# Kernel tuning notes

Measured on AMD Instinct MI355X. Metric: run time of the kernel, lower is better.

The kernel has to match this reference:

```python
import jax, jax.numpy as jnp
import numpy as np

EMB = 4096   # emb_size for c2=256 (per TransformerEncoderBlock mapping)
HEADS = 16
HDIM = EMB // HEADS  # 256
N = 25               # (h // (h//5))**2 patches
PATCH = 4            # h//5 with h=20
C = 256
HW = 20
LN_EPS = 1e-5


def _layernorm(x, g, b):
    m = jnp.mean(x, axis=-1, keepdims=True)
    v = jnp.var(x, axis=-1, keepdims=True)
    return (x - m) * jax.lax.rsqrt(v + LN_EPS) * g + b


def setup_inputs() -> dict:
    key = jax.random.key(0)
    ks = jax.random.split(key, 14)
    s = 0.02
    rn = lambda k, shape, sc=s: jax.random.normal(k, shape, jnp.float32) * sc
    return {
        "x": jax.random.normal(ks[0], (1, C, HW, HW), jnp.float32),
        # PatchEmbedding: Conv2d(C, EMB, k=4, s=4) + positions
        "pe_w": rn(ks[1], (EMB, C, PATCH, PATCH)),
        "pe_b": jnp.zeros((EMB,), jnp.float32),
        "pos": rn(ks[2], (N, EMB), 1.0),  # nn.Parameter(torch.randn(...))
        # shared LayerNorm (same module used twice per block)
        "ln_g": jnp.ones((EMB,), jnp.float32),
        "ln_b": jnp.zeros((EMB,), jnp.float32),
        # attention
        "qkv_w": rn(ks[3], (EMB, 3 * EMB)),
        "qkv_b": jnp.zeros((3 * EMB,), jnp.float32),
        "proj_w": rn(ks[4], (EMB, EMB)),
        "proj_b": jnp.zeros((EMB,), jnp.float32),
        # FFN (expansion 4)
        "ff1_w": rn(ks[5], (EMB, 4 * EMB)),
        "ff1_b": jnp.zeros((4 * EMB,), jnp.float32),
        "ff2_w": rn(ks[6], (4 * EMB, EMB)),
        "ff2_b": jnp.zeros((EMB,), jnp.float32),
    }


def _forward(x, pe_w, pe_b, pos, ln_g, ln_b, qkv_w, qkv_b, proj_w, proj_b,
             ff1_w, ff1_b, ff2_w, ff2_b):
    b = x.shape[0]
    # Patch embedding: Conv2d(k=4, s=4) -> [b, EMB, 5, 5] -> [b, 25, EMB]
    t = jax.lax.conv_general_dilated(
        x, pe_w, window_strides=(PATCH, PATCH), padding="VALID",
        dimension_numbers=("NCHW", "OIHW", "NCHW"))
    t = t + pe_b[None, :, None, None]
    t = t.reshape(b, EMB, N).transpose(0, 2, 1) + pos  # [b, N, EMB]

    # --- TransformerEncoderBlock (dropout inactive / eval mode) ---
    # attention branch
    h = _layernorm(t, ln_g, ln_b)
    qkv = (h @ qkv_w + qkv_b).reshape(b, N, HEADS, HDIM, 3)  # (h d qkv) split
    q = qkv[..., 0].transpose(0, 2, 1, 3)  # [b, H, N, D]
    k = qkv[..., 1].transpose(0, 2, 1, 3)
    v = qkv[..., 2].transpose(0, 2, 1, 3)
    energy = jnp.einsum("bhqd,bhkd->bhqk", q, k)
    # NOTE: original scales AFTER softmax by sqrt(emb_size) -- faithful copy
    att = jax.nn.softmax(energy, axis=-1) / (EMB ** 0.5)
    o = jnp.einsum("bhqk,bhkd->bhqd", att, v)
    o = o.transpose(0, 2, 1, 3).reshape(b, N, EMB)
    t = t + (o @ proj_w + proj_b)

    # FFN branch (same shared layernorm params)
    h = _layernorm(t, ln_g, ln_b)
    h = jax.nn.gelu(h @ ff1_w + ff1_b, approximate=False)  # torch nn.GELU exact
    t = t + (h @ ff2_w + ff2_b)

    # final reshape(1, c2, w, h)
    return t.reshape(1, C, HW, HW)


def reference(x, pe_w, pe_b, pos, ln_g, ln_b, qkv_w, qkv_b, proj_w, proj_b,
              ff1_w, ff1_b, ff2_w, ff2_b):
    return _forward(x, pe_w, pe_b, pos, ln_g, ln_b, qkv_w, qkv_b, proj_w,
                    proj_b, ff1_w, ff1_b, ff2_w, ff2_b)
```

## Files before the change

kernel.cpp:

```cpp
#include <hip/hip_runtime.h>
#include <math.h>

#define TOK 25

typedef __attribute__((ext_vector_type(8))) short short8_t;
typedef __attribute__((ext_vector_type(4))) float f32x4_t;

__device__ __forceinline__ short bf16r(float f) {
  union { float f; unsigned u; } v;
  v.f = f;
  unsigned r = v.u + 0x7FFFu + ((v.u >> 16) & 1u);
  return (short)(r >> 16);
}
__device__ __forceinline__ unsigned packbf2(float lo, float hi) {
  return ((unsigned)(unsigned short)bf16r(hi) << 16) |
         (unsigned short)bf16r(lo);
}

__global__ __launch_bounds__(256) void k_patchify(const float* __restrict__ x,
                                                  unsigned short* __restrict__ P) {
  int idx = blockIdx.x * 256 + threadIdx.x;
  int n = idx >> 12;
  int rem = idx & 4095;
  int c = rem >> 4;
  int kh = (rem >> 2) & 3;
  int kw = rem & 3;
  int py = n / 5, px = n - py * 5;
  P[idx] = (unsigned short)bf16r(x[c * 400 + (py * 4 + kh) * 20 + (px * 4 + kw)]);
}

template <int KC, int WT>
__global__ __launch_bounds__(256) void k_mfma(
    const unsigned short* __restrict__ A, const float* __restrict__ W,
    float* __restrict__ part, int K, int N) {
  constexpr int LDA = KC + 8;
  __shared__ __align__(16) unsigned short As[TOK * LDA];
  const int tid = threadIdx.x;
  const int lane = tid & 63;
  const int lm = lane & 15;
  const int lg = lane >> 4;
  const int wv = tid >> 6;
  const int s = blockIdx.y;
  const int k0 = s * KC;
  const int c0 = blockIdx.x * 256 + wv * 64;
  for (int i = tid; i < TOK * (KC / 8); i += 256) {
    int r = i / (KC / 8);
    int o = i - r * (KC / 8);
    uint4 v = *reinterpret_cast<const uint4*>(A + (long)r * K + k0 + o * 8);
    *reinterpret_cast<uint4*>(&As[r * LDA + o * 8]) = v;
  }
  __syncthreads();
  const int r1 = 16 + lm;
  const int r1c = (r1 < TOK) ? r1 : 0;
  f32x4_t acc[4][2];
#pragma unroll
  for (int g = 0; g < 4; ++g) {
    acc[g][0] = (f32x4_t){0.f, 0.f, 0.f, 0.f};
    acc[g][1] = (f32x4_t){0.f, 0.f, 0.f, 0.f};
  }
  for (int ks = 0; ks < KC; ks += 32) {
    const int kb = k0 + ks + lg * 8;
    float bf[4][8];
    if (WT == 0) {
      const float* bp = W + (long)kb * N + c0 + lm;
#pragma unroll
      for (int j = 0; j < 8; ++j) {
        const float* bj = bp + (long)j * N;
#pragma unroll
        for (int g = 0; g < 4; ++g) bf[g][j] = bj[g * 16];
      }
    } else {
#pragma unroll
      for (int g = 0; g < 4; ++g) {
        const float* bp = W + (long)(c0 + g * 16 + lm) * K + kb;
        float4 b0 = *reinterpret_cast<const float4*>(bp);
        float4 b1 = *reinterpret_cast<const float4*>(bp + 4);
        bf[g][0] = b0.x; bf[g][1] = b0.y; bf[g][2] = b0.z; bf[g][3] = b0.w;
        bf[g][4] = b1.x; bf[g][5] = b1.y; bf[g][6] = b1.z; bf[g][7] = b1.w;
      }
    }
    short8_t av0 =
        *reinterpret_cast<const short8_t*>(&As[lm * LDA + ks + lg * 8]);
    short8_t av1 =
        *reinterpret_cast<const short8_t*>(&As[r1c * LDA + ks + lg * 8]);
#pragma unroll
    for (int g = 0; g < 4; ++g) {
      short8_t bv;
#pragma unroll
      for (int j = 0; j < 8; ++j) bv[j] = bf16r(bf[g][j]);
      acc[g][0] = __builtin_amdgcn_mfma_f32_16x16x32_bf16(av0, bv, acc[g][0], 0, 0, 0);
      acc[g][1] = __builtin_amdgcn_mfma_f32_16x16x32_bf16(av1, bv, acc[g][1], 0, 0, 0);
    }
  }
  float* pp = part + ((long)s * TOK) * N + c0 + lm;
#pragma unroll
  for (int g = 0; g < 4; ++g) {
    float* pg = pp + g * 16;
#pragma unroll
    for (int r = 0; r < 4; ++r) {
      int row0 = lg * 4 + r;
      pg[(long)row0 * N] = acc[g][0][r];
      int row1 = 16 + lg * 4 + r;
      if (row1 < TOK) pg[(long)row1 * N] = acc[g][1][r];
    }
  }
}

template <int S, int GELU, int RES, int OBF>
__global__ __launch_bounds__(256) void k_reduce(const float* __restrict__ part,
                                                const float* __restrict__ bias,
                                                const float* __restrict__ res,
                                                void* __restrict__ outv,
                                                int Nout) {
  long idx4 = (long)blockIdx.x * 256 + threadIdx.x;
  int c4 = (int)(idx4 % (Nout >> 2));
  const long stride4 = (long)TOK * (Nout >> 2);
  const float4* p4 = reinterpret_cast<const float4*>(part) + idx4;
  float4 v = {0.f, 0.f, 0.f, 0.f};
#pragma unroll
  for (int s = 0; s < S; ++s) {
    float4 t = p4[s * stride4];
    v.x += t.x; v.y += t.y; v.z += t.z; v.w += t.w;
  }
  float4 bb = reinterpret_cast<const float4*>(bias)[c4];
  v.x += bb.x; v.y += bb.y; v.z += bb.z; v.w += bb.w;
  if (GELU) {
    v.x = 0.5f * v.x * (1.f + erff(v.x * 0.70710678118654752f));
    v.y = 0.5f * v.y * (1.f + erff(v.y * 0.70710678118654752f));
    v.z = 0.5f * v.z * (1.f + erff(v.z * 0.70710678118654752f));
    v.w = 0.5f * v.w * (1.f + erff(v.w * 0.70710678118654752f));
  }
  if (RES) {
    float4 rr = reinterpret_cast<const float4*>(res)[idx4];
    v.x += rr.x; v.y += rr.y; v.z += rr.z; v.w += rr.w;
  }
  if (OBF) {
    uint2 o;
    o.x = packbf2(v.x, v.y);
    o.y = packbf2(v.z, v.w);
    reinterpret_cast<uint2*>(outv)[idx4] = o;
  } else {
    reinterpret_cast<float4*>(outv)[idx4] = v;
  }
}

__global__ __launch_bounds__(256) void k_ln(const float* __restrict__ t,
                                            const float* __restrict__ g,
                                            const float* __restrict__ b,
                                            unsigned short* __restrict__ h) {
  const int n = blockIdx.x;
  const float4* row = reinterpret_cast<const float4*>(t + n * 4096);
  float s = 0.f, s2 = 0.f;
  float4 vbuf[4];
#pragma unroll
  for (int it = 0; it < 4; ++it) {
    float4 v = row[threadIdx.x + it * 256];
    vbuf[it] = v;
    s += v.x + v.y + v.z + v.w;
    s2 += v.x * v.x + v.y * v.y + v.z * v.z + v.w * v.w;
  }
#pragma unroll
  for (int off = 32; off >= 1; off >>= 1) {
    s += __shfl_down(s, off);
    s2 += __shfl_down(s2, off);
  }
  __shared__ float red[8];
  if ((threadIdx.x & 63) == 0) {
    red[threadIdx.x >> 6] = s;
    red[4 + (threadIdx.x >> 6)] = s2;
  }
  __syncthreads();
  float st = red[0] + red[1] + red[2] + red[3];
  float s2t = red[4] + red[5] + red[6] + red[7];
  float mean = st * (1.f / 4096.f);
  float var = s2t * (1.f / 4096.f) - mean * mean;
  float rstd = rsqrtf(var + 1e-5f);
  const float4* g4 = reinterpret_cast<const float4*>(g);
  const float4* b4 = reinterpret_cast<const float4*>(b);
  uint2* h2 = reinterpret_cast<uint2*>(h) + (long)n * 1024;
#pragma unroll
  for (int it = 0; it < 4; ++it) {
    int i = threadIdx.x + it * 256;
    float4 v = vbuf[it];
    float4 gg = g4[i];
    float4 bb = b4[i];
    float4 o;
    o.x = (v.x - mean) * rstd * gg.x + bb.x;
    o.y = (v.y - mean) * rstd * gg.y + bb.y;
    o.z = (v.z - mean) * rstd * gg.z + bb.z;
    o.w = (v.w - mean) * rstd * gg.w + bb.w;
    uint2 pk;
    pk.x = packbf2(o.x, o.y);
    pk.y = packbf2(o.z, o.w);
    h2[i] = pk;
  }
}

__global__ __launch_bounds__(256) void k_attn_qk(const float* __restrict__ qkv,
                                                 float* __restrict__ att) {
  const int head = blockIdx.x;
  __shared__ float q[TOK][260];
  __shared__ float k[TOK][260];
  __shared__ float e[TOK][TOK];
  const int d = threadIdx.x;
#pragma unroll
  for (int n = 0; n < TOK; ++n) {
    const long base = (long)n * 12288 + (head * 256 + d) * 3;
    q[n][d] = qkv[base];
    k[n][d] = qkv[base + 1];
  }
  __syncthreads();
  for (int p = threadIdx.x; p < TOK * TOK; p += 256) {
    int i = p / TOK, j = p - i * TOK;
    float acc = 0.f;
#pragma unroll
    for (int kk = 0; kk < 256; kk += 4) {
      float4 a = *reinterpret_cast<const float4*>(&q[i][kk]);
      float4 bb = *reinterpret_cast<const float4*>(&k[j][kk]);
      acc = fmaf(a.x, bb.x, acc);
      acc = fmaf(a.y, bb.y, acc);
      acc = fmaf(a.z, bb.z, acc);
      acc = fmaf(a.w, bb.w, acc);
    }
    e[i][j] = acc;
  }
  __syncthreads();
  if (threadIdx.x < TOK) {
    const int i = threadIdx.x;
    float m = -1e30f;
    for (int j = 0; j < TOK; ++j) m = fmaxf(m, e[i][j]);
    float ssum = 0.f;
    float ex[TOK];
#pragma unroll
    for (int j = 0; j < TOK; ++j) {
      ex[j] = expf(e[i][j] - m);
      ssum += ex[j];
    }
    float inv = 1.f / (ssum * 64.f);
#pragma unroll
    for (int j = 0; j < TOK; ++j) att[head * 625 + i * TOK + j] = ex[j] * inv;
  }
}

__global__ __launch_bounds__(256) void k_attn_pv(const float* __restrict__ qkv,
                                                 const float* __restrict__ att,
                                                 unsigned short* __restrict__ o) {
  const int head = blockIdx.x;
  const int d = threadIdx.x;
  __shared__ float a[TOK * TOK];
  for (int i = threadIdx.x; i < TOK * TOK; i += 256) a[i] = att[head * 625 + i];
  __syncthreads();
  float acc[TOK];
#pragma unroll
  for (int i = 0; i < TOK; ++i) acc[i] = 0.f;
#pragma unroll
  for (int j = 0; j < TOK; ++j) {
    float vv = qkv[(long)j * 12288 + (head * 256 + d) * 3 + 2];
#pragma unroll
    for (int i = 0; i < TOK; ++i) acc[i] = fmaf(a[i * TOK + j], vv, acc[i]);
  }
#pragma unroll
  for (int i = 0; i < TOK; ++i)
    o[(long)i * 4096 + head * 256 + d] = (unsigned short)bf16r(acc[i]);
}

extern "C" void kernel_launch(void* const* d_in, const int* in_sizes, int n_in,
                              void* d_out, int out_size, void* d_ws, size_t ws_size,
                              hipStream_t stream) {
  (void)in_sizes; (void)n_in; (void)out_size; (void)ws_size;
  const float* x      = (const float*)d_in[0];
  const float* pe_w   = (const float*)d_in[1];
  const float* pe_b   = (const float*)d_in[2];
  const float* pos    = (const float*)d_in[3];
  const float* ln_g   = (const float*)d_in[4];
  const float* ln_b   = (const float*)d_in[5];
  const float* qkv_w  = (const float*)d_in[6];
  const float* qkv_b  = (const float*)d_in[7];
  const float* proj_w = (const float*)d_in[8];
  const float* proj_b = (const float*)d_in[9];
  const float* ff1_w  = (const float*)d_in[10];
  const float* ff1_b  = (const float*)d_in[11];
  const float* ff2_w  = (const float*)d_in[12];
  const float* ff2_b  = (const float*)d_in[13];
  float* out = (float*)d_out;

  float* ws = (float*)d_ws;
  unsigned short* P_bf = (unsigned short*)ws;
  float* T    = ws + 102400;
  unsigned short* H_bf = (unsigned short*)(ws + 204800);
  float* QKV  = ws + 307200;
  unsigned short* O_bf = (unsigned short*)(ws + 614400);
  unsigned short* G_bf = (unsigned short*)(ws + 716800);
  float* ATT  = ws + 1126400;
  float* PART = ws + 1136400;

  k_patchify<<<400, 256, 0, stream>>>(x, P_bf);
  k_mfma<128, 1><<<dim3(16, 32), 256, 0, stream>>>(P_bf, pe_w, PART, 4096, 4096);
  k_reduce<32, 0, 1, 0><<<100, 256, 0, stream>>>(PART, pe_b, pos, T, 4096);
  k_ln<<<25, 256, 0, stream>>>(T, ln_g, ln_b, H_bf);

  k_mfma<256, 0><<<dim3(48, 16), 256, 0, stream>>>(H_bf, qkv_w, PART, 4096, 12288);
  k_reduce<16, 0, 0, 0><<<300, 256, 0, stream>>>(PART, qkv_b, nullptr, QKV, 12288);
  k_attn_qk<<<16, 256, 0, stream>>>(QKV, ATT);
  k_attn_pv<<<16, 256, 0, stream>>>(QKV, ATT, O_bf);
  k_mfma<128, 0><<<dim3(16, 32), 256, 0, stream>>>(O_bf, proj_w, PART, 4096, 4096);
  k_reduce<32, 0, 1, 0><<<100, 256, 0, stream>>>(PART, proj_b, T, T, 4096);
  k_ln<<<25, 256, 0, stream>>>(T, ln_g, ln_b, H_bf);

  k_mfma<256, 0><<<dim3(64, 16), 256, 0, stream>>>(H_bf, ff1_w, PART, 4096, 16384);
  k_reduce<16, 1, 0, 1><<<400, 256, 0, stream>>>(PART, ff1_b, nullptr, G_bf, 16384);
  k_mfma<512, 0><<<dim3(16, 32), 256, 0, stream>>>(G_bf, ff2_w, PART, 16384, 4096);
  k_reduce<32, 0, 1, 0><<<100, 256, 0, stream>>>(PART, ff2_b, T, out, 4096);
}
```

Before: 252.2 us.

## Fuse patchify into patch-embed GEMM, merge attention kernels, use hardware bf16 converts

Removes the separate patchify kernel. The patch-embedding GEMM now gathers input pixels straight from x into shared memory as bf16. The QK/softmax and PV attention kernels are merged into one kernel that keeps the attention matrix in shared memory, which drops a launch and a global round trip. Manual bit-twiddling bf16 rounding is replaced by compiler vector conversions, which may map to native convert instructions and cut ALU work in the GEMM inner loop.

Result: faster. 243.3 us (-3.5%).

```diff
diff --git a/kernel.cpp b/kernel.cpp
--- a/kernel.cpp
+++ b/kernel.cpp
@@ -5,28 +5,20 @@
 
 typedef __attribute__((ext_vector_type(8))) short short8_t;
 typedef __attribute__((ext_vector_type(4))) float f32x4_t;
-
-__device__ __forceinline__ short bf16r(float f) {
-  union { float f; unsigned u; } v;
-  v.f = f;
-  unsigned r = v.u + 0x7FFFu + ((v.u >> 16) & 1u);
-  return (short)(r >> 16);
-}
-__device__ __forceinline__ unsigned packbf2(float lo, float hi) {
-  return ((unsigned)(unsigned short)bf16r(hi) << 16) |
-         (unsigned short)bf16r(lo);
-}
-
-__global__ __launch_bounds__(256) void k_patchify(const float* __restrict__ x,
-                                                  unsigned short* __restrict__ P) {
-  int idx = blockIdx.x * 256 + threadIdx.x;
-  int n = idx >> 12;
-  int rem = idx & 4095;
-  int c = rem >> 4;
-  int kh = (rem >> 2) & 3;
-  int kw = rem & 3;
-  int py = n / 5, px = n - py * 5;
-  P[idx] = (unsigned short)bf16r(x[c * 400 + (py * 4 + kh) * 20 + (px * 4 + kw)]);
+typedef __attribute__((ext_vector_type(8))) float floatx8;
+typedef __attribute__((ext_vector_type(4))) float floatx4;
+typedef __attribute__((ext_vector_type(8))) __bf16 bf16x8_t;
+typedef __attribute__((ext_vector_type(4))) __bf16 bf16x4_t;
+
+__device__ __forceinline__ short8_t cvt8(floatx8 f) {
+  return __builtin_bit_cast(short8_t, __builtin_convertvector(f, bf16x8_t));
+}
+__device__ __forceinline__ uint2 cvt4pack(float4 v) {
+  floatx4 f = {v.x, v.y, v.z, v.w};
+  return __builtin_bit_cast(uint2, __builtin_convertvector(f, bf16x4_t));
+}
+__device__ __forceinline__ unsigned short bf1(float f) {
+  return __builtin_bit_cast(unsigned short, (__bf16)f);
 }
 
 template <int KC, int WT>
@@ -60,14 +52,14 @@
   }
   for (int ks = 0; ks < KC; ks += 32) {
     const int kb = k0 + ks + lg * 8;
-    float bf[4][8];
+    floatx8 bfv[4];
     if (WT == 0) {
       const float* bp = W + (long)kb * N + c0 + lm;
 #pragma unroll
       for (int j = 0; j < 8; ++j) {
         const float* bj = bp + (long)j * N;
 #pragma unroll
-        for (int g = 0; g < 4; ++g) bf[g][j] = bj[g * 16];
+        for (int g = 0; g < 4; ++g) bfv[g][j] = bj[g * 16];
       }
     } else {
 #pragma unroll
@@ -75,8 +67,7 @@
         const float* bp = W + (long)(c0 + g * 16 + lm) * K + kb;
         float4 b0 = *reinterpret_cast<const float4*>(bp);
         float4 b1 = *reinterpret_cast<const float4*>(bp + 4);
-        bf[g][0] = b0.x; bf[g][1] = b0.y; bf[g][2] = b0.z; bf[g][3] = b0.w;
-        bf[g][4] = b1.x; bf[g][5] = b1.y; bf[g][6] = b1.z; bf[g][7] = b1.w;
+        bfv[g] = (floatx8){b0.x, b0.y, b0.z, b0.w, b1.x, b1.y, b1.z, b1.w};
       }
     }
     short8_t av0 =
@@ -85,9 +76,79 @@
         *reinterpret_cast<const short8_t*>(&As[r1c * LDA + ks + lg * 8]);
 #pragma unroll
     for (int g = 0; g < 4; ++g) {
-      short8_t bv;
-#pragma unroll
-      for (int j = 0; j < 8; ++j) bv[j] = bf16r(bf[g][j]);
+      short8_t bv = cvt8(bfv[g]);
+      acc[g][0] = __builtin_amdgcn_mfma_f32_16x16x32_bf16(av0, bv, acc[g][0], 0, 0, 0);
+      acc[g][1] = __builtin_amdgcn_mfma_f32_16x16x32_bf16(av1, bv, acc[g][1], 0, 0, 0);
+    }
+  }
+  float* pp = part + ((long)s * TOK) * N + c0 + lm;
+#pragma unroll
+  for (int g = 0; g < 4; ++g) {
+    float* pg = pp + g * 16;
+#pragma unroll
+    for (int r = 0; r < 4; ++r) {
+      int row0 = lg * 4 + r;
+      pg[(long)row0 * N] = acc[g][0][r];
+      int row1 = 16 + lg * 4 + r;
+      if (row1 < TOK) pg[(long)row1 * N] = acc[g][1][r];
+    }
+  }
+}
+
+template <int KC>
+__global__ __launch_bounds__(256) void k_mfma_pe(
+    const float* __restrict__ x, const float* __restrict__ W,
+    float* __restrict__ part, int K, int N) {
+  constexpr int LDA = KC + 8;
+  __shared__ __align__(16) unsigned short As[TOK * LDA];
+  const int tid = threadIdx.x;
+  const int lane = tid & 63;
+  const int lm = lane & 15;
+  const int lg = lane >> 4;
+  const int wv = tid >> 6;
+  const int s = blockIdx.y;
+  const int k0 = s * KC;
+  const int c0 = blockIdx.x * 256 + wv * 64;
+  for (int i = tid; i < TOK * (KC / 8); i += 256) {
+    int r = i / (KC / 8);
+    int o = i - r * (KC / 8);
+    int kb = k0 + o * 8;
+    int c = kb >> 4;
+    int kh0 = (kb >> 2) & 3;
+    int py = r / 5, px = r - py * 5;
+    const float* xp = x + c * 400 + (py * 4 + kh0) * 20 + px * 4;
+    float4 lo = *reinterpret_cast<const float4*>(xp);
+    float4 hi = *reinterpret_cast<const float4*>(xp + 20);
+    floatx8 f = {lo.x, lo.y, lo.z, lo.w, hi.x, hi.y, hi.z, hi.w};
+    short8_t v = cvt8(f);
+    *reinterpret_cast<short8_t*>(&As[r * LDA + o * 8]) = v;
+  }
+  __syncthreads();
+  const int r1 = 16 + lm;
+  const int r1c = (r1 < TOK) ? r1 : 0;
+  f32x4_t acc[4][2];
+#pragma unroll
+  for (int g = 0; g < 4; ++g) {
+    acc[g][0] = (f32x4_t){0.f, 0.f, 0.f, 0.f};
+    acc[g][1] = (f32x4_t){0.f, 0.f, 0.f, 0.f};
+  }
+  for (int ks = 0; ks < KC; ks += 32) {
+    const int kb = k0 + ks + lg * 8;
+    floatx8 bfv[4];
+#pragma unroll
+    for (int g = 0; g < 4; ++g) {
+      const float* bp = W + (long)(c0 + g * 16 + lm) * K + kb;
+      float4 b0 = *reinterpret_cast<const float4*>(bp);
+      float4 b1 = *reinterpret_cast<const float4*>(bp + 4);
+      bfv[g] = (floatx8){b0.x, b0.y, b0.z, b0.w, b1.x, b1.y, b1.z, b1.w};
+    }
+    short8_t av0 =
+        *reinterpret_cast<const short8_t*>(&As[lm * LDA + ks + lg * 8]);
+    short8_t av1 =
+        *reinterpret_cast<const short8_t*>(&As[r1c * LDA + ks + lg * 8]);
+#pragma unroll
+    for (int g = 0; g < 4; ++g) {
+      short8_t bv = cvt8(bfv[g]);
       acc[g][0] = __builtin_amdgcn_mfma_f32_16x16x32_bf16(av0, bv, acc[g][0], 0, 0, 0);
       acc[g][1] = __builtin_amdgcn_mfma_f32_16x16x32_bf16(av1, bv, acc[g][1], 0, 0, 0);
     }
@@ -135,10 +196,7 @@
     v.x += rr.x; v.y += rr.y; v.z += rr.z; v.w += rr.w;
   }
   if (OBF) {
-    uint2 o;
-    o.x = packbf2(v.x, v.y);
-    o.y = packbf2(v.z, v.w);
-    reinterpret_cast<uint2*>(outv)[idx4] = o;
+    reinterpret_cast<uint2*>(outv)[idx4] = cvt4pack(v);
   } else {
     reinterpret_cast<float4*>(outv)[idx4] = v;
   }
@@ -189,66 +247,54 @@
     o.y = (v.y - mean) * rstd * gg.y + bb.y;
     o.z = (v.z - mean) * rstd * gg.z + bb.z;
     o.w = (v.w - mean) * rstd * gg.w + bb.w;
-    uint2 pk;
-    pk.x = packbf2(o.x, o.y);
-    pk.y = packbf2(o.z, o.w);
-    h2[i] = pk;
-  }
-}
-
-__global__ __launch_bounds__(256) void k_attn_qk(const float* __restrict__ qkv,
-                                                 float* __restrict__ att) {
+    h2[i] = cvt4pack(o);
+  }
+}
+
+__global__ __launch_bounds__(256) void k_attn(const float* __restrict__ qkv,
+                                              unsigned short* __restrict__ o) {
   const int head = blockIdx.x;
   __shared__ float q[TOK][260];
-  __shared__ float k[TOK][260];
-  __shared__ float e[TOK][TOK];
+  __shared__ float kk[TOK][260];
+  __shared__ float att[TOK][TOK];
   const int d = threadIdx.x;
 #pragma unroll
   for (int n = 0; n < TOK; ++n) {
     const long base = (long)n * 12288 + (head * 256 + d) * 3;
     q[n][d] = qkv[base];
-    k[n][d] = qkv[base + 1];
+    kk[n][d] = qkv[base + 1];
   }
   __syncthreads();
   for (int p = threadIdx.x; p < TOK * TOK; p += 256) {
     int i = p / TOK, j = p - i * TOK;
     float acc = 0.f;
 #pragma unroll
-    for (int kk = 0; kk < 256; kk += 4) {
-      float4 a = *reinterpret_cast<const float4*>(&q[i][kk]);
-      float4 bb = *reinterpret_cast<const float4*>(&k[j][kk]);
+    for (int c = 0; c < 256; c += 4) {
+      float4 a = *reinterpret_cast<const float4*>(&q[i][c]);
+      float4 bb = *reinterpret_cast<const float4*>(&kk[j][c]);
       acc = fmaf(a.x, bb.x, acc);
       acc = fmaf(a.y, bb.y, acc);
       acc = fmaf(a.z, bb.z, acc);
       acc = fmaf(a.w, bb.w, acc);
     }
-    e[i][j] = acc;
+    att[i][j] = acc;
   }
   __syncthreads();
   if (threadIdx.x < TOK) {
     const int i = threadIdx.x;
     float m = -1e30f;
-    for (int j = 0; j < TOK; ++j) m = fmaxf(m, e[i][j]);
+    for (int j = 0; j < TOK; ++j) m = fmaxf(m, att[i][j]);
     float ssum = 0.f;
     float ex[TOK];
 #pragma unroll
     for (int j = 0; j < TOK; ++j) {
-      ex[j] = expf(e[i][j] - m);
+      ex[j] = expf(att[i][j] - m);
       ssum += ex[j];
     }
     float inv = 1.f / (ssum * 64.f);
 #pragma unroll
-    for (int j = 0; j < TOK; ++j) att[head * 625 + i * TOK + j] = ex[j] * inv;
-  }
-}
-
-__global__ __launch_bounds__(256) void k_attn_pv(const float* __restrict__ qkv,
-                                                 const float* __restrict__ att,
-                                                 unsigned short* __restrict__ o) {
-  const int head = blockIdx.x;
-  const int d = threadIdx.x;
-  __shared__ float a[TOK * TOK];
-  for (int i = threadIdx.x; i < TOK * TOK; i += 256) a[i] = att[head * 625 + i];
+    for (int j = 0; j < TOK; ++j) att[i][j] = ex[j] * inv;
+  }
   __syncthreads();
   float acc[TOK];
 #pragma unroll
@@ -257,11 +303,11 @@
   for (int j = 0; j < TOK; ++j) {
     float vv = qkv[(long)j * 12288 + (head * 256 + d) * 3 + 2];
 #pragma unroll
-    for (int i = 0; i < TOK; ++i) acc[i] = fmaf(a[i * TOK + j], vv, acc[i]);
+    for (int i = 0; i < TOK; ++i) acc[i] = fmaf(att[i][j], vv, acc[i]);
   }
 #pragma unroll
   for (int i = 0; i < TOK; ++i)
-    o[(long)i * 4096 + head * 256 + d] = (unsigned short)bf16r(acc[i]);
+    o[(long)i * 4096 + head * 256 + d] = bf1(acc[i]);
 }
 
 extern "C" void kernel_launch(void* const* d_in, const int* in_sizes, int n_in,
@@ -285,24 +331,20 @@
   float* out = (float*)d_out;
 
   float* ws = (float*)d_ws;
-  unsigned short* P_bf = (unsigned short*)ws;
   float* T    = ws + 102400;
   unsigned short* H_bf = (unsigned short*)(ws + 204800);
   float* QKV  = ws + 307200;
   unsigned short* O_bf = (unsigned short*)(ws + 614400);
   unsigned short* G_bf = (unsigned short*)(ws + 716800);
-  float* ATT  = ws + 1126400;
   float* PART = ws + 1136400;
 
-  k_patchify<<<400, 256, 0, stream>>>(x, P_bf);
-  k_mfma<128, 1><<<dim3(16, 32), 256, 0, stream>>>(P_bf, pe_w, PART, 4096, 4096);
+  k_mfma_pe<128><<<dim3(16, 32), 256, 0, stream>>>(x, pe_w, PART, 4096, 4096);
   k_reduce<32, 0, 1, 0><<<100, 256, 0, stream>>>(PART, pe_b, pos, T, 4096);
   k_ln<<<25, 256, 0, stream>>>(T, ln_g, ln_b, H_bf);
 
   k_mfma<256, 0><<<dim3(48, 16), 256, 0, stream>>>(H_bf, qkv_w, PART, 4096, 12288);
   k_reduce<16, 0, 0, 0><<<300, 256, 0, stream>>>(PART, qkv_b, nullptr, QKV, 12288);
-  k_attn_qk<<<16, 256, 0, stream>>>(QKV, ATT);
-  k_attn_pv<<<16, 256, 0, stream>>>(QKV, ATT, O_bf);
+  k_attn<<<16, 256, 0, stream>>>(QKV, O_bf);
   k_mfma<128, 0><<<dim3(16, 32), 256, 0, stream>>>(O_bf, proj_w, PART, 4096, 4096);
   k_reduce<32, 0, 1, 0><<<100, 256, 0, stream>>>(PART, proj_b, T, T, 4096);
   k_ln<<<25, 256, 0, stream>>>(T, ln_g, ln_b, H_bf);
```
